# Kernel tuning notes

Hardware: AMD Instinct MI355X
Metric: run time of the kernel (lower is better)

## Reference

```python
import jax, jax.numpy as jnp
import numpy as np

LAYERS = 5      # lstm_layers
H = 1           # lstm_hidden_size
IN = 21         # 9 (rot) + 6 (v) + 6 (u)
NEG = 0.1       # LeakyReLU negative slope
EPS = 1e-5      # BatchNorm1d eps


def _lstm_cell(x, h, c, w_ih, w_hh):
    # torch gate order: i, f, g, o ; no biases (lstm_bias=False)
    gates = x @ w_ih.T + h @ w_hh.T              # [k, 4H]
    i, f, g, o = jnp.split(gates, 4, axis=-1)
    i = jax.nn.sigmoid(i)
    f = jax.nn.sigmoid(f)
    g = jnp.tanh(g)
    o = jax.nn.sigmoid(o)
    c_new = f * c + i * g
    h_new = o * jnp.tanh(c_new)
    return h_new, c_new


def _bn_train(z, gamma, beta):
    # BatchNorm1d in training mode: batch stats, biased variance
    m = z.mean(axis=0)
    var = z.var(axis=0)
    return gamma * (z - m) / jnp.sqrt(var + EPS) + beta


def setup_inputs() -> dict:
    key = jax.random.key(0)
    ks = jax.random.split(key, 14)
    k, T = 65536, 32
    s = 0.2  # init scale, roughly torch uniform(-1/sqrt(H)) magnitude
    inp = {
        "r": jax.random.normal(ks[0], (k, T, 9), jnp.float32),
        "v": jax.random.normal(ks[1], (k, T, 6), jnp.float32),
        "u": jax.random.normal(ks[2], (k, T, 6), jnp.float32),
        # LSTM weights: layer 0 sees IN features, layers 1..4 see H
        "w_ih0": jax.random.normal(ks[3], (4 * H, IN), jnp.float32) * s,
        "w_ih_rest": jax.random.normal(ks[4], (LAYERS - 1, 4 * H, H), jnp.float32) * s,
        "w_hh": jax.random.normal(ks[5], (LAYERS, 4 * H, H), jnp.float32) * s,
        # FC head: Linear(H,32,no bias) -> BN -> LReLU -> Linear(32,32) -> BN -> LReLU -> Linear(32,6)
        "W1": jax.random.normal(ks[6], (32, H), jnp.float32) * s,
        "g1": jnp.ones((32,), jnp.float32),
        "b1": jnp.zeros((32,), jnp.float32),
        "W2": jax.random.normal(ks[7], (32, 32), jnp.float32) * s,
        "g2": jnp.ones((32,), jnp.float32),
        "b2": jnp.zeros((32,), jnp.float32),
        "W3": jax.random.normal(ks[8], (6, 32), jnp.float32) * s,
    }
    return inp


def reference(r, v, u, w_ih0, w_ih_rest, w_hh, W1, g1, b1, W2, g2, b2, W3):
    x = jnp.concatenate([r, v, u], axis=-1)          # [k, T, 21]
    k = x.shape[0]
    h0 = jnp.zeros((LAYERS, k, H), x.dtype)
    c0 = jnp.zeros((LAYERS, k, H), x.dtype)
    xs = jnp.swapaxes(x, 0, 1)                       # [T, k, 21]

    def step(carry, xt):
        h, c = carry
        hs, cs = [], []
        layer_in = xt
        for l in range(LAYERS):
            w_ih = w_ih0 if l == 0 else w_ih_rest[l - 1]
            hl, cl = _lstm_cell(layer_in, h[l], c[l], w_ih, w_hh[l])
            hs.append(hl)
            cs.append(cl)
            layer_in = hl
        return (jnp.stack(hs), jnp.stack(cs)), layer_in  # top-layer output

    (hT, cT), outs = jax.lax.scan(step, (h0, c0), xs)    # outs: [T, k, H]

    # fc applied to out[:, 0] -> first timestep of top layer
    y = outs[0]                                          # [k, H]
    y = jax.nn.leaky_relu(_bn_train(y @ W1.T, g1, b1), NEG)
    y = jax.nn.leaky_relu(_bn_train(y @ W2.T, g2, b2), NEG)
    dv = y @ W3.T                                        # [k, 6]
    return dv[:, None], hT, cT
```

## Files before the change

### kernel.cpp

```cpp
#include <hip/hip_runtime.h>
#include <math.h>

#define T 32
#define NEGS 0.1f
#define EPS 1e-5f
#define NREG 33


__device__ __forceinline__ float rcp_fast(float x) { return __builtin_amdgcn_rcpf(x); }
__device__ __forceinline__ float sigm(float x) { return rcp_fast(1.0f + __expf(-x)); }
__device__ __forceinline__ float tanh_fast(float x) {
    float t = __expf(2.0f * fabsf(x));
    float r = 1.0f - 2.0f * rcp_fast(t + 1.0f);
    return copysignf(r, x);
}
__device__ __forceinline__ float lrelu(float x) { return x > 0.0f ? x : NEGS * x; }

__device__ __forceinline__ void bn1_params(const float* __restrict__ W1,
                                           const float* __restrict__ g1,
                                           const float* __restrict__ b1,
                                           const double* __restrict__ wsd, int k, int j,
                                           float& my, float& vy, float& a, float& b,
                                           float& tau, int& flip)
{
    my = (float)(wsd[0] / k);
    vy = (float)(wsd[1] / k) - my * my;
    float wj = W1[j];
    a = g1[j] * wj * rsqrtf(fmaf(wj * wj, vy, EPS));
    b = b1[j];
    if (a > 0.0f)      { tau = my - b / a; flip = 0; }
    else if (a < 0.0f) { tau = my - b / a; flip = 1; }
    else               { tau = (b > 0.0f ? -__builtin_inff() : __builtin_inff()); flip = 0; }
}

__global__ __launch_bounds__(256)
void gates_kernel(const float* __restrict__ r, const float* __restrict__ v,
                  const float* __restrict__ u, const float* __restrict__ wih0,
                  float4* __restrict__ xg, int k)
{
    __shared__ float rbuf[8 * 32 * 9];
    __shared__ float vbuf[8 * 32 * 6];
    __shared__ float ubuf[8 * 32 * 6];
    __shared__ float obuf[32 * 36];
    const int tid = threadIdx.x;
    const int s0 = blockIdx.x * 8;

    const float4* r4 = reinterpret_cast<const float4*>(r + (size_t)s0 * (T * 9));
    const float4* v4 = reinterpret_cast<const float4*>(v + (size_t)s0 * (T * 6));
    const float4* u4 = reinterpret_cast<const float4*>(u + (size_t)s0 * (T * 6));
    float4* rb4 = reinterpret_cast<float4*>(rbuf);
    float4* vb4 = reinterpret_cast<float4*>(vbuf);
    float4* ub4 = reinterpret_cast<float4*>(ubuf);

    rb4[tid] = r4[tid];
    rb4[256 + tid] = r4[256 + tid];
    if (tid < 64) rb4[512 + tid] = r4[512 + tid];
    vb4[tid] = v4[tid];
    if (tid < 128) vb4[256 + tid] = v4[256 + tid];
    ub4[tid] = u4[tid];
    if (tid < 128) ub4[256 + tid] = u4[256 + tid];

    float wi0[4][21];
#pragma unroll
    for (int g = 0; g < 4; ++g)
#pragma unroll
        for (int j = 0; j < 21; ++j) wi0[g][j] = wih0[g * 21 + j];

    __syncthreads();

    const int sl = tid >> 5, t = tid & 31;
    float x[21];
#pragma unroll
    for (int j = 0; j < 9; ++j) x[j] = rbuf[sl * (32 * 9) + t * 9 + j];
#pragma unroll
    for (int j = 0; j < 6; ++j) x[9 + j] = vbuf[sl * (32 * 6) + t * 6 + j];
#pragma unroll
    for (int j = 0; j < 6; ++j) x[15 + j] = ubuf[sl * (32 * 6) + t * 6 + j];

    float4 g4;
    float* gp = (float*)&g4;
#pragma unroll
    for (int g = 0; g < 4; ++g) {
        float acc = 0.f;
#pragma unroll
        for (int j = 0; j < 21; ++j) acc = fmaf(wi0[g][j], x[j], acc);
        gp[g] = acc;
    }
    *(float4*)&obuf[t * 36 + sl * 4] = g4;
    __syncthreads();

    const int tG = tid >> 3, j = tid & 7;
    float4 val = *(const float4*)&obuf[tG * 36 + j * 4];
    xg[(size_t)tG * k + s0 + j] = val;
}

__global__ __launch_bounds__(256, 1)
void recur_kernel(const float4* __restrict__ xg, const float* __restrict__ wihr,
                  const float* __restrict__ whhp, float* __restrict__ out,
                  double* __restrict__ wsd, float* __restrict__ wsy, int k)
{
    const int s = blockIdx.x * 256 + threadIdx.x;

    float4 gbuf[T];
#pragma unroll
    for (int t = 0; t < T; ++t) gbuf[t] = xg[(size_t)t * k + s];

    float wir[4][4];
#pragma unroll
    for (int l = 0; l < 4; ++l)
#pragma unroll
        for (int g = 0; g < 4; ++g) wir[l][g] = wihr[l * 4 + g];
    float whh[5][4];
#pragma unroll
    for (int l = 0; l < 5; ++l)
#pragma unroll
        for (int g = 0; g < 4; ++g) whh[l][g] = whhp[l * 4 + g];

    asm volatile("" ::: "memory");

    float h[5] = {0.f, 0.f, 0.f, 0.f, 0.f};
    float c[5] = {0.f, 0.f, 0.f, 0.f, 0.f};
    float y0 = 0.f;

#pragma unroll
    for (int t = 0; t < T; ++t) {
        const float4 G = gbuf[t];
        float a0 = fmaf(whh[0][0], h[0], G.x);
        float a1 = fmaf(whh[0][1], h[0], G.y);
        float a2 = fmaf(whh[0][2], h[0], G.z);
        float a3 = fmaf(whh[0][3], h[0], G.w);
        {
            float ii = sigm(a0), ff = sigm(a1);
            float gg = tanh_fast(a2), oo = sigm(a3);
            c[0] = ff * c[0] + ii * gg;
            h[0] = oo * tanh_fast(c[0]);
        }
        float xin = h[0];
#pragma unroll
        for (int l = 1; l < 5; ++l) {
            float b0 = fmaf(wir[l - 1][0], xin, whh[l][0] * h[l]);
            float b1 = fmaf(wir[l - 1][1], xin, whh[l][1] * h[l]);
            float b2 = fmaf(wir[l - 1][2], xin, whh[l][2] * h[l]);
            float b3 = fmaf(wir[l - 1][3], xin, whh[l][3] * h[l]);
            float ii = sigm(b0), ff = sigm(b1);
            float gg = tanh_fast(b2), oo = sigm(b3);
            c[l] = ff * c[l] + ii * gg;
            h[l] = oo * tanh_fast(c[l]);
            xin = h[l];
        }
        if (t == 0) y0 = h[4];
    }

#pragma unroll
    for (int l = 0; l < 5; ++l) {
        out[(size_t)6 * k + (size_t)l * k + s] = h[l];
        out[(size_t)11 * k + (size_t)l * k + s] = c[l];
    }
    wsy[s] = y0;

    float ys = y0, yq = y0 * y0;
#pragma unroll
    for (int off = 32; off; off >>= 1) {
        ys += __shfl_down(ys, off);
        yq += __shfl_down(yq, off);
    }
    __shared__ float pS[4], pQ[4];
    const int wid = threadIdx.x >> 6, lane = threadIdx.x & 63;
    if (lane == 0) { pS[wid] = ys; pQ[wid] = yq; }
    __syncthreads();
    if (threadIdx.x == 0) {
        atomicAdd(&wsd[0], (double)(pS[0] + pS[1] + pS[2] + pS[3]));
        atomicAdd(&wsd[1], (double)(pQ[0] + pQ[1] + pQ[2] + pQ[3]));
    }
}

__global__ __launch_bounds__(256, 1)
void lstm_fused(const float* __restrict__ r, const float* __restrict__ v,
                const float* __restrict__ u,
                const float* __restrict__ wih0, const float* __restrict__ wihr,
                const float* __restrict__ whhp,
                float* __restrict__ out, double* __restrict__ wsd,
                float* __restrict__ wsy, int k)
{
    const int s = blockIdx.x * 256 + threadIdx.x;
    float wi0[4][21];
#pragma unroll
    for (int g = 0; g < 4; ++g)
#pragma unroll
        for (int j = 0; j < 21; ++j) wi0[g][j] = wih0[g * 21 + j];
    float wir[4][4];
#pragma unroll
    for (int l = 0; l < 4; ++l)
#pragma unroll
        for (int g = 0; g < 4; ++g) wir[l][g] = wihr[l * 4 + g];
    float whh[5][4];
#pragma unroll
    for (int l = 0; l < 5; ++l)
#pragma unroll
        for (int g = 0; g < 4; ++g) whh[l][g] = whhp[l * 4 + g];

    const float4* r4 = reinterpret_cast<const float4*>(r + (size_t)s * (T * 9));
    const float4* v4 = reinterpret_cast<const float4*>(v + (size_t)s * (T * 6));
    const float4* u4 = reinterpret_cast<const float4*>(u + (size_t)s * (T * 6));

    float h[5] = {0.f, 0.f, 0.f, 0.f, 0.f};
    float c[5] = {0.f, 0.f, 0.f, 0.f, 0.f};
    float y0 = 0.f;

    for (int t0 = 0; t0 < T; t0 += 4) {
        const int cb = t0 >> 2;
        float4 rb[9], vb[6], ub[6];
#pragma unroll
        for (int q = 0; q < 9; ++q) rb[q] = r4[cb * 9 + q];
#pragma unroll
        for (int q = 0; q < 6; ++q) vb[q] = v4[cb * 6 + q];
#pragma unroll
        for (int q = 0; q < 6; ++q) ub[q] = u4[cb * 6 + q];
        float rf[36], vf[24], uf[24];
#pragma unroll
        for (int q = 0; q < 9; ++q) {
            rf[4 * q] = rb[q].x; rf[4 * q + 1] = rb[q].y;
            rf[4 * q + 2] = rb[q].z; rf[4 * q + 3] = rb[q].w;
        }
#pragma unroll
        for (int q = 0; q < 6; ++q) {
            vf[4 * q] = vb[q].x; vf[4 * q + 1] = vb[q].y;
            vf[4 * q + 2] = vb[q].z; vf[4 * q + 3] = vb[q].w;
            uf[4 * q] = ub[q].x; uf[4 * q + 1] = ub[q].y;
            uf[4 * q + 2] = ub[q].z; uf[4 * q + 3] = ub[q].w;
        }
#pragma unroll
        for (int dt = 0; dt < 4; ++dt) {
            float x[21];
#pragma unroll
            for (int j = 0; j < 9; ++j) x[j] = rf[dt * 9 + j];
#pragma unroll
            for (int j = 0; j < 6; ++j) x[9 + j] = vf[dt * 6 + j];
#pragma unroll
            for (int j = 0; j < 6; ++j) x[15 + j] = uf[dt * 6 + j];
            float gt[4];
#pragma unroll
            for (int g = 0; g < 4; ++g) {
                float a = whh[0][g] * h[0];
#pragma unroll
                for (int j = 0; j < 21; ++j) a = fmaf(wi0[g][j], x[j], a);
                gt[g] = a;
            }
            {
                float ii = sigm(gt[0]), ff = sigm(gt[1]);
                float gg = tanh_fast(gt[2]), oo = sigm(gt[3]);
                c[0] = ff * c[0] + ii * gg;
                h[0] = oo * tanh_fast(c[0]);
            }
            float xin = h[0];
#pragma unroll
            for (int l = 1; l < 5; ++l) {
                float b0 = fmaf(wir[l - 1][0], xin, whh[l][0] * h[l]);
                float b1 = fmaf(wir[l - 1][1], xin, whh[l][1] * h[l]);
                float b2 = fmaf(wir[l - 1][2], xin, whh[l][2] * h[l]);
                float b3 = fmaf(wir[l - 1][3], xin, whh[l][3] * h[l]);
                float ii = sigm(b0), ff = sigm(b1);
                float gg = tanh_fast(b2), oo = sigm(b3);
                c[l] = ff * c[l] + ii * gg;
                h[l] = oo * tanh_fast(c[l]);
                xin = h[l];
            }
            if (t0 + dt == 0) y0 = h[4];
        }
    }
#pragma unroll
    for (int l = 0; l < 5; ++l) {
        out[(size_t)6 * k + (size_t)l * k + s] = h[l];
        out[(size_t)11 * k + (size_t)l * k + s] = c[l];
    }
    wsy[s] = y0;
    float ys = y0, yq = y0 * y0;
#pragma unroll
    for (int off = 32; off; off >>= 1) {
        ys += __shfl_down(ys, off);
        yq += __shfl_down(yq, off);
    }
    __shared__ float pS[4], pQ[4];
    const int wid = threadIdx.x >> 6, lane = threadIdx.x & 63;
    if (lane == 0) { pS[wid] = ys; pQ[wid] = yq; }
    __syncthreads();
    if (threadIdx.x == 0) {
        atomicAdd(&wsd[0], (double)(pS[0] + pS[1] + pS[2] + pS[3]));
        atomicAdd(&wsd[1], (double)(pQ[0] + pQ[1] + pQ[2] + pQ[3]));
    }
}

__global__ __launch_bounds__(256)
void hist_kernel(const float* __restrict__ W1, const float* __restrict__ g1,
                 const float* __restrict__ b1, double* __restrict__ wsd,
                 const float* __restrict__ wsy, int k)
{
    __shared__ float sTau[32];
    __shared__ float sH[3 * NREG];
    __shared__ float sMy;
    const int tid = threadIdx.x;
    if (tid < 3 * NREG) sH[tid] = 0.f;
    if (tid < 32) {
        float my, vy, a, b, tau; int flip;
        bn1_params(W1, g1, b1, wsd, k, tid, my, vy, a, b, tau, flip);
        sTau[tid] = tau;
        if (tid == 0) sMy = my;
    }
    __syncthreads();
    const int stride = gridDim.x * 256;
    for (int s = blockIdx.x * 256 + tid; s < k; s += stride) {
        const float y = wsy[s];
        const float yc = y - sMy;
        int rgn = 0;
#pragma unroll
        for (int j = 0; j < 32; ++j) rgn += (y > sTau[j]) ? 1 : 0;
        atomicAdd(&sH[rgn], 1.0f);
        atomicAdd(&sH[NREG + rgn], yc);
        atomicAdd(&sH[2 * NREG + rgn], yc * yc);
    }
    __syncthreads();
    if (tid < 3 * NREG) atomicAdd(&wsd[2 + tid], (double)sH[tid]);
}

__global__ __launch_bounds__(256)
void tables_kernel(const float* __restrict__ W1, const float* __restrict__ g1,
                   const float* __restrict__ b1, const float* __restrict__ W2,
                   const float* __restrict__ g2, const float* __restrict__ b2,
                   const double* __restrict__ wsd, float* __restrict__ gPQ, int k)
{
    __shared__ float sA[32], sB[32], sTau[32];
    __shared__ int sRank[32], sFlip[32];
    __shared__ float sS0[NREG], sS1[NREG], sS2[NREG];
    __shared__ float sW2[1024];
    __shared__ float sSumY1[32];
    __shared__ float sM[1024];
    __shared__ float sI2[32], sM2v[32], sB2[32];
    const int tid = threadIdx.x;

    for (int i = tid; i < 1024; i += 256) sW2[i] = W2[i];
    if (tid < NREG) {
        sS0[tid] = (float)wsd[2 + tid];
        sS1[tid] = (float)wsd[2 + NREG + tid];
        sS2[tid] = (float)wsd[2 + 2 * NREG + tid];
    }
    if (tid < 32) {
        float my, vy, a, b, tau; int flip;
        bn1_params(W1, g1, b1, wsd, k, tid, my, vy, a, b, tau, flip);
        sA[tid] = a; sB[tid] = b; sTau[tid] = tau; sFlip[tid] = flip;
        sB2[tid] = b2[tid];
    }
    __syncthreads();
    if (tid < 32) {
        int rk = 0;
        float tj = sTau[tid];
#pragma unroll
        for (int l = 0; l < 32; ++l)
            rk += (sTau[l] < tj || (sTau[l] == tj && l < tid)) ? 1 : 0;
        sRank[tid] = rk;
    }
    __syncthreads();
    if (tid < 32) {
        const int rk = sRank[tid], fl = sFlip[tid];
        const float a = sA[tid], b = sB[tid];
        float acc = 0.f;
        for (int rg = 0; rg < NREG; ++rg) {
            float m = (((rk < rg) ? 1 : 0) != fl) ? 1.0f : NEGS;
            acc += m * (a * sS1[rg] + b * sS0[rg]);
        }
        sSumY1[tid] = acc;
    }
    for (int p = tid; p < 1024; p += 256) {
        const int j = p >> 5, l = p & 31;
        const int rj = sRank[j], fj = sFlip[j];
        const int rl = sRank[l], flp = sFlip[l];
        const float aj = sA[j], bj = sB[j], al = sA[l], bl = sB[l];
        const float caa = aj * al, cab = aj * bl + al * bj, cbb = bj * bl;
        float acc = 0.f;
        for (int rg = 0; rg < NREG; ++rg) {
            float mj = (((rj < rg) ? 1 : 0) != fj) ? 1.0f : NEGS;
            float ml = (((rl < rg) ? 1 : 0) != flp) ? 1.0f : NEGS;
            acc += mj * ml * (caa * sS2[rg] + cab * sS1[rg] + cbb * sS0[rg]);
        }
        sM[p] = acc;
    }
    __syncthreads();
    if (tid < 32) {
        const int i = tid;
        float s2 = 0.f, ss2 = 0.f;
#pragma unroll
        for (int j = 0; j < 32; ++j) {
            float wij = sW2[i * 32 + j];
            s2 = fmaf(wij, sSumY1[j], s2);
            float tj = 0.f;
#pragma unroll
            for (int l = 0; l < 32; ++l) tj = fmaf(sW2[i * 32 + l], sM[j * 32 + l], tj);
            ss2 = fmaf(wij, tj, ss2);
        }
        float m2 = s2 / k;
        float v2 = ss2 / k - m2 * m2;
        sM2v[i] = m2;
        sI2[i] = g2[i] * rsqrtf(v2 + EPS);
    }
    __syncthreads();
    for (int idx = tid; idx < NREG * 32; idx += 256) {
        const int rg = idx >> 5, i = idx & 31;
        float Ai = 0.f, Bi = 0.f;
#pragma unroll
        for (int j = 0; j < 32; ++j) {
            float m = (((sRank[j] < rg) ? 1 : 0) != sFlip[j]) ? 1.0f : NEGS;
            float w = sW2[i * 32 + j] * m;
            Ai = fmaf(w, sA[j], Ai);
            Bi = fmaf(w, sB[j], Bi);
        }
        gPQ[idx] = sI2[i] * Ai;
        gPQ[NREG * 32 + idx] = sI2[i] * (Bi - sM2v[i]) + sB2[i];
    }
}

__global__ __launch_bounds__(256)
void final_kernel(const float* __restrict__ W1, const float* __restrict__ g1,
                  const float* __restrict__ b1, const float* __restrict__ W3,
                  const double* __restrict__ wsd, const float* __restrict__ wsy,
                  const float* __restrict__ gPQ, float* __restrict__ out, int k)
{
    __shared__ float sTau[32], sW3[192], sMy;
    __shared__ float sP[NREG][33], sQ[NREG][33];
    const int tid = threadIdx.x;
    for (int idx = tid; idx < NREG * 32; idx += 256) {
        const int rg = idx >> 5, i = idx & 31;
        sP[rg][i] = gPQ[idx];
        sQ[rg][i] = gPQ[NREG * 32 + idx];
    }
    if (tid < 192) sW3[tid] = W3[tid];
    if (tid < 32) {
        float my, vy, a, b, tau; int flip;
        bn1_params(W1, g1, b1, wsd, k, tid, my, vy, a, b, tau, flip);
        sTau[tid] = tau;
        if (tid == 0) sMy = my;
    }
    __syncthreads();
    const int s = blockIdx.x * 256 + tid;
    const float y = wsy[s];
    const float yc = y - sMy;
    int rgn = 0;
#pragma unroll
    for (int j = 0; j < 32; ++j) rgn += (y > sTau[j]) ? 1 : 0;
    float dv[6] = {0.f, 0.f, 0.f, 0.f, 0.f, 0.f};
#pragma unroll
    for (int i = 0; i < 32; ++i) {
        float y2 = lrelu(fmaf(sP[rgn][i], yc, sQ[rgn][i]));
#pragma unroll
        for (int m = 0; m < 6; ++m) dv[m] = fmaf(sW3[m * 32 + i], y2, dv[m]);
    }
#pragma unroll
    for (int m = 0; m < 6; ++m) out[(size_t)s * 6 + m] = dv[m];
}

extern "C" void kernel_launch(void* const* d_in, const int* in_sizes, int n_in,
                              void* d_out, int out_size, void* d_ws, size_t ws_size,
                              hipStream_t stream)
{
    const float* r    = (const float*)d_in[0];
    const float* v    = (const float*)d_in[1];
    const float* u    = (const float*)d_in[2];
    const float* wih0 = (const float*)d_in[3];
    const float* wihr = (const float*)d_in[4];
    const float* whhp = (const float*)d_in[5];
    const float* W1   = (const float*)d_in[6];
    const float* g1v  = (const float*)d_in[7];
    const float* b1v  = (const float*)d_in[8];
    const float* W2   = (const float*)d_in[9];
    const float* g2v  = (const float*)d_in[10];
    const float* b2v  = (const float*)d_in[11];
    const float* W3   = (const float*)d_in[12];

    const int k = in_sizes[0] / (T * 9);
    float* out = (float*)d_out;
    double* wsd = (double*)d_ws;
    float* wsy = (float*)((char*)d_ws + 1024);

    const size_t xg_off = 1024 + (size_t)k * 4;
    const size_t need = xg_off + (size_t)k * T * 16 + (size_t)NREG * 32 * 2 * 4;

    hipMemsetAsync(d_ws, 0, 1024, stream);

    const int blocks = k / 256;
    float* gPQ;
    if (ws_size >= need) {
        float4* xg = (float4*)((char*)d_ws + xg_off);
        gPQ = (float*)((char*)d_ws + xg_off + (size_t)k * T * 16);
        gates_kernel<<<k / 8, 256, 0, stream>>>(r, v, u, wih0, xg, k);
        recur_kernel<<<blocks, 256, 0, stream>>>(xg, wihr, whhp, out, wsd, wsy, k);
    } else {
        gPQ = (float*)((char*)d_ws + xg_off);
        lstm_fused<<<blocks, 256, 0, stream>>>(r, v, u, wih0, wihr, whhp, out, wsd, wsy, k);
    }
    hist_kernel<<<64, 256, 0, stream>>>(W1, g1v, b1v, wsd, wsy, k);
    tables_kernel<<<1, 256, 0, stream>>>(W1, g1v, b1v, W2, g2v, b2v, wsd, gPQ, k);
    final_kernel<<<blocks, 256, 0, stream>>>(W1, g1v, b1v, W3, wsd, wsy, gPQ, out, k);
}
```

Baseline: 259.6 us.

## Make gates kernel persistent with register-prefetched next group loads

The gates kernel becomes a grid-stride persistent kernel capped at 1536 blocks. Each block prefetches the next 8-sample group's r/v/u data into registers while it computes the current group from shared memory. This is meant to overlap global load latency with compute and to cut block launch overhead compared with launching 8192 blocks. In exchange, register pressure rises from holding the prefetched float4 values, and with fewer blocks resident per CU there may be less latency hiding.

```diff
diff --git a/kernel.cpp b/kernel.cpp
--- a/kernel.cpp
+++ b/kernel.cpp
@@ -36,62 +36,87 @@
 __global__ __launch_bounds__(256)
 void gates_kernel(const float* __restrict__ r, const float* __restrict__ v,
                   const float* __restrict__ u, const float* __restrict__ wih0,
-                  float4* __restrict__ xg, int k)
+                  float4* __restrict__ xg, int k, int ngroups)
 {
     __shared__ float rbuf[8 * 32 * 9];
     __shared__ float vbuf[8 * 32 * 6];
     __shared__ float ubuf[8 * 32 * 6];
     __shared__ float obuf[32 * 36];
     const int tid = threadIdx.x;
-    const int s0 = blockIdx.x * 8;
-
-    const float4* r4 = reinterpret_cast<const float4*>(r + (size_t)s0 * (T * 9));
-    const float4* v4 = reinterpret_cast<const float4*>(v + (size_t)s0 * (T * 6));
-    const float4* u4 = reinterpret_cast<const float4*>(u + (size_t)s0 * (T * 6));
+
     float4* rb4 = reinterpret_cast<float4*>(rbuf);
     float4* vb4 = reinterpret_cast<float4*>(vbuf);
     float4* ub4 = reinterpret_cast<float4*>(ubuf);
 
-    rb4[tid] = r4[tid];
-    rb4[256 + tid] = r4[256 + tid];
-    if (tid < 64) rb4[512 + tid] = r4[512 + tid];
-    vb4[tid] = v4[tid];
-    if (tid < 128) vb4[256 + tid] = v4[256 + tid];
-    ub4[tid] = u4[tid];
-    if (tid < 128) ub4[256 + tid] = u4[256 + tid];
-
     float wi0[4][21];
 #pragma unroll
     for (int g = 0; g < 4; ++g)
 #pragma unroll
         for (int j = 0; j < 21; ++j) wi0[g][j] = wih0[g * 21 + j];
 
-    __syncthreads();
-
-    const int sl = tid >> 5, t = tid & 31;
-    float x[21];
-#pragma unroll
-    for (int j = 0; j < 9; ++j) x[j] = rbuf[sl * (32 * 9) + t * 9 + j];
-#pragma unroll
-    for (int j = 0; j < 6; ++j) x[9 + j] = vbuf[sl * (32 * 6) + t * 6 + j];
-#pragma unroll
-    for (int j = 0; j < 6; ++j) x[15 + j] = ubuf[sl * (32 * 6) + t * 6 + j];
-
-    float4 g4;
-    float* gp = (float*)&g4;
-#pragma unroll
-    for (int g = 0; g < 4; ++g) {
-        float acc = 0.f;
-#pragma unroll
-        for (int j = 0; j < 21; ++j) acc = fmaf(wi0[g][j], x[j], acc);
-        gp[g] = acc;
-    }
-    *(float4*)&obuf[t * 36 + sl * 4] = g4;
-    __syncthreads();
-
-    const int tG = tid >> 3, j = tid & 7;
-    float4 val = *(const float4*)&obuf[tG * 36 + j * 4];
-    xg[(size_t)tG * k + s0 + j] = val;
+    float4 Ra0, Ra1, Ra2, Rv0, Rv1, Ru0, Ru1;
+
+#define ISSUE_GROUP(gg)                                                         \
+    do {                                                                        \
+        const float4* r4_ = reinterpret_cast<const float4*>(r + (size_t)(gg) * (8 * T * 9)); \
+        const float4* v4_ = reinterpret_cast<const float4*>(v + (size_t)(gg) * (8 * T * 6)); \
+        const float4* u4_ = reinterpret_cast<const float4*>(u + (size_t)(gg) * (8 * T * 6)); \
+        Ra0 = r4_[tid];                                                         \
+        Ra1 = r4_[256 + tid];                                                   \
+        if (tid < 64) Ra2 = r4_[512 + tid];                                     \
+        Rv0 = v4_[tid];                                                         \
+        if (tid < 128) Rv1 = v4_[256 + tid];                                    \
+        Ru0 = u4_[tid];                                                         \
+        if (tid < 128) Ru1 = u4_[256 + tid];                                    \
+    } while (0)
+
+    int g = blockIdx.x;
+    const int gstride = gridDim.x;
+    if (g >= ngroups) return;
+    ISSUE_GROUP(g);
+
+    while (g < ngroups) {
+        rb4[tid] = Ra0;
+        rb4[256 + tid] = Ra1;
+        if (tid < 64) rb4[512 + tid] = Ra2;
+        vb4[tid] = Rv0;
+        if (tid < 128) vb4[256 + tid] = Rv1;
+        ub4[tid] = Ru0;
+        if (tid < 128) ub4[256 + tid] = Ru1;
+
+        const int gn = g + gstride;
+        if (gn < ngroups) ISSUE_GROUP(gn);
+
+        __syncthreads();
+
+        const int sl = tid >> 5, t = tid & 31;
+        float x[21];
+#pragma unroll
+        for (int j = 0; j < 9; ++j) x[j] = rbuf[sl * (32 * 9) + t * 9 + j];
+#pragma unroll
+        for (int j = 0; j < 6; ++j) x[9 + j] = vbuf[sl * (32 * 6) + t * 6 + j];
+#pragma unroll
+        for (int j = 0; j < 6; ++j) x[15 + j] = ubuf[sl * (32 * 6) + t * 6 + j];
+
+        float4 g4;
+        float* gp = (float*)&g4;
+#pragma unroll
+        for (int gi = 0; gi < 4; ++gi) {
+            float acc = 0.f;
+#pragma unroll
+            for (int j = 0; j < 21; ++j) acc = fmaf(wi0[gi][j], x[j], acc);
+            gp[gi] = acc;
+        }
+        *(float4*)&obuf[t * 36 + sl * 4] = g4;
+        __syncthreads();
+
+        const int tG = tid >> 3, j = tid & 7;
+        float4 val = *(const float4*)&obuf[tG * 36 + j * 4];
+        xg[(size_t)tG * k + g * 8 + j] = val;
+
+        g = gn;
+    }
+#undef ISSUE_GROUP
 }
 
 __global__ __launch_bounds__(256, 1)
@@ -489,7 +514,10 @@
     if (ws_size >= need) {
         float4* xg = (float4*)((char*)d_ws + xg_off);
         gPQ = (float*)((char*)d_ws + xg_off + (size_t)k * T * 16);
-        gates_kernel<<<k / 8, 256, 0, stream>>>(r, v, u, wih0, xg, k);
+        const int ngroups = k / 8;
+        int pblocks = 1536;
+        if (pblocks > ngroups) pblocks = ngroups;
+        gates_kernel<<<pblocks, 256, 0, stream>>>(r, v, u, wih0, xg, k, ngroups);
         recur_kernel<<<blocks, 256, 0, stream>>>(xg, wihr, whhp, out, wsd, wsy, k);
     } else {
         gPQ = (float*)((char*)d_ws + xg_off);
```

Result: slower. 266.6 us (+2.7%).
